# Performance work log

Measured on AMD Instinct MI355X. Metric: run time of the kernel, lower is better.

## Reference

```python
import jax, jax.numpy as jnp
import numpy as np

N_NODES = 100000
N_EDGES = 1200000
IN_CH = 64
HID = 64


def sage_conv(x, src, dst, Wl, b, Wr, num_nodes):
    # mean aggregation of source-node features at target nodes (flow=source_to_target)
    msg = x[src]                                      # [E, C] gather
    agg = jax.ops.segment_sum(msg, dst, num_segments=num_nodes)  # [N, C]
    cnt = jax.ops.segment_sum(jnp.ones((src.shape[0],), x.dtype), dst,
                              num_segments=num_nodes)
    mean = agg / jnp.maximum(cnt, 1.0)[:, None]
    # PyG SAGEConv: lin_l(aggregated) + bias + lin_r(root)
    return mean @ Wl + b + x @ Wr


def setup_inputs() -> dict:
    key = jax.random.key(0)
    ks = jax.random.split(key, 10)
    x = jax.random.normal(ks[0], (N_NODES, IN_CH), dtype=jnp.float32)
    edge_index = jax.random.randint(ks[1], (2, N_EDGES), 0, N_NODES, dtype=jnp.int64)
    s1 = 1.0 / np.sqrt(IN_CH)
    s2 = 1.0 / np.sqrt(HID)
    W1l = jax.random.uniform(ks[2], (IN_CH, HID), jnp.float32, -s1, s1)
    b1 = jax.random.uniform(ks[3], (HID,), jnp.float32, -s1, s1)
    W1r = jax.random.uniform(ks[4], (IN_CH, HID), jnp.float32, -s1, s1)
    W2l = jax.random.uniform(ks[5], (HID, HID), jnp.float32, -s2, s2)
    b2 = jax.random.uniform(ks[6], (HID,), jnp.float32, -s2, s2)
    W2r = jax.random.uniform(ks[7], (HID, HID), jnp.float32, -s2, s2)
    Wfc = jax.random.uniform(ks[8], (HID, 1), jnp.float32, -s2, s2)
    bfc = jax.random.uniform(ks[9], (1,), jnp.float32, -s2, s2)
    return {"x": x, "edge_index": edge_index, "W1l": W1l, "b1": b1, "W1r": W1r,
            "W2l": W2l, "b2": b2, "W2r": W2r, "Wfc": Wfc, "bfc": bfc}


def reference(x, edge_index, W1l, b1, W1r, W2l, b2, W2r, Wfc, bfc):
    num_nodes = x.shape[0]
    src, dst = edge_index[0], edge_index[1]
    x = jnp.nan_to_num(x, nan=0.0)
    # layer 1: SAGEConv -> ReLU (dropout is identity in eval)
    h = jax.nn.relu(sage_conv(x, src, dst, W1l, b1, W1r, num_nodes))
    # layer 2
    h = jax.nn.relu(sage_conv(h, src, dst, W2l, b2, W2r, num_nodes))
    pred = (h @ Wfc + bfc)[:, 0]  # (num_nodes,)
    return pred
```

## Files before the change

### kernel.cpp

```cpp
#include <hip/hip_runtime.h>

#define NN_NODES 100000
#define NN_EDGES 1200000
#define CH 64
#define BUCKET_NODES 200
#define NBUCKETS (NN_NODES / BUCKET_NODES)
#define EPB 4096
#define PREP_THREADS 1024
#define XCDS 8
#define PCAP 768
#define BMAX (XCDS * PCAP)

#define PA_BLOCKS ((NN_EDGES + EPB - 1) / EPB)
#define CV_ITEMS (NN_NODES * CH / 4)
#define CV_BLOCKS ((CV_ITEMS + PREP_THREADS - 1) / PREP_THREADS)
#define WP_ITEMS (64 * 128)
#define WP_BLOCKS ((WP_ITEMS + PREP_THREADS - 1) / PREP_THREADS)

#define FUSED_NODES 16
#define FUSED_BLOCKS (NN_NODES / FUSED_NODES)

typedef __attribute__((ext_vector_type(8))) short bf16x8;
typedef __attribute__((ext_vector_type(4))) float f32x4;

__device__ __forceinline__ float nan0(float v) { return v == v ? v : 0.0f; }

__device__ __forceinline__ unsigned short f2bf(float f) {
    unsigned u = __float_as_uint(f);
    return (unsigned short)((u + 0x7fffu + ((u >> 16) & 1u)) >> 16);
}

__device__ __forceinline__ unsigned xcc_id() {
    unsigned x;
    asm volatile("s_getreg_b32 %0, hwreg(HW_REG_XCC_ID)" : "=s"(x));
    return x & (XCDS - 1);
}

__global__ __launch_bounds__(PREP_THREADS) void prep_kernel(
    const float* __restrict__ x, unsigned short* __restrict__ xb,
    const float* __restrict__ W1l, const float* __restrict__ W1r,
    const float* __restrict__ W2l, const float* __restrict__ W2r,
    unsigned short* __restrict__ Wt1, unsigned short* __restrict__ Wt2,
    const int* __restrict__ src, const int* __restrict__ dst,
    int* __restrict__ bcnt, unsigned int* __restrict__ bbuf)
{
    __shared__ int lhist[NBUCKETS];
    __shared__ int lbase[NBUCKETS];
    int tid = threadIdx.x;
    int bid = blockIdx.x;

    if (bid < PA_BLOCKS) {
        int e0 = bid * EPB;
        unsigned xcc = xcc_id();

        for (int i = tid; i < NBUCKETS; i += PREP_THREADS) lhist[i] = 0;
        __syncthreads();

        int eb = e0 + tid * 4;
        int nv = NN_EDGES - eb;
        if (nv > 4) nv = 4;
        int da[4] = {-1, -1, -1, -1};
        if (nv == 4) {
            int4 dv = *(const int4*)(dst + eb);
            da[0] = dv.x; da[1] = dv.y; da[2] = dv.z; da[3] = dv.w;
        } else {
            for (int r = 0; r < nv; r++) da[r] = dst[eb + r];
        }
        #pragma unroll
        for (int r = 0; r < 4; r++)
            if (da[r] >= 0) atomicAdd(&lhist[da[r] / BUCKET_NODES], 1);
        __syncthreads();

        for (int i = tid; i < NBUCKETS; i += PREP_THREADS) {
            int c = lhist[i];
            lbase[i] = c > 0 ? atomicAdd(&bcnt[i * XCDS + xcc], c) : 0;
            lhist[i] = 0;
        }
        __syncthreads();

        int sa[4] = {0, 0, 0, 0};
        if (nv == 4) {
            int4 sv = *(const int4*)(src + eb);
            sa[0] = sv.x; sa[1] = sv.y; sa[2] = sv.z; sa[3] = sv.w;
        } else {
            for (int r = 0; r < nv; r++) sa[r] = src[eb + r];
        }
        #pragma unroll
        for (int r = 0; r < 4; r++) {
            int d = da[r];
            if (d >= 0) {
                int b = d / BUCKET_NODES;
                int dloc = d - b * BUCKET_NODES;
                int pos = lbase[b] + atomicAdd(&lhist[b], 1);
                if (pos < PCAP)
                    bbuf[((size_t)b * XCDS + xcc) * PCAP + pos] =
                        ((unsigned)dloc << 24) | (unsigned)sa[r];
            }
        }
    } else if (bid < PA_BLOCKS + CV_BLOCKS) {
        int i = (bid - PA_BLOCKS) * PREP_THREADS + tid;
        if (i < CV_ITEMS) {
            float4 v = ((const float4*)x)[i];
            v.x = nan0(v.x); v.y = nan0(v.y); v.z = nan0(v.z); v.w = nan0(v.w);
            ushort4 o;
            o.x = f2bf(v.x); o.y = f2bf(v.y); o.z = f2bf(v.z); o.w = f2bf(v.w);
            ((ushort4*)xb)[i] = o;
        }
    } else {
        int i = (bid - PA_BLOCKS - CV_BLOCKS) * PREP_THREADS + tid;
        if (i < WP_ITEMS) {
            int n = i >> 7;
            int k = i & 127;
            float v1 = (k < 64) ? W1l[k * 64 + n] : W1r[(k - 64) * 64 + n];
            float v2 = (k < 64) ? W2l[k * 64 + n] : W2r[(k - 64) * 64 + n];
            Wt1[i] = f2bf(v1);
            Wt2[i] = f2bf(v2);
        }
    }
}

__global__ __launch_bounds__(256) void passB_kernel(
    const int* __restrict__ bcnt, const unsigned int* __restrict__ bbuf,
    int* __restrict__ col, int* __restrict__ rowptr)
{
    __shared__ int hist[BUCKET_NODES];
    __shared__ int cur[BUCKET_NODES];
    __shared__ int sc[256];
    __shared__ unsigned int stage[BMAX];
    int b = blockIdx.x;
    int t = threadIdx.x;

    for (int i = t; i < BUCKET_NODES; i += 256) hist[i] = 0;

    int part = 0;
    int lim = b * XCDS;
    for (int i = t; i < lim; i += 256) {
        int c = bcnt[i];
        part += c > PCAP ? PCAP : c;
    }
    sc[t] = part;
    __syncthreads();
    #pragma unroll
    for (int off = 128; off > 0; off >>= 1) {
        if (t < off) sc[t] += sc[t + off];
        __syncthreads();
    }
    int base = sc[0];
    __syncthreads();

    int cnt = 0;
    #pragma unroll
    for (int x = 0; x < XCDS; x++) {
        int pc = bcnt[b * XCDS + x];
        if (pc > PCAP) pc = PCAP;
        const unsigned int* seg = bbuf + ((size_t)b * XCDS + x) * PCAP;
        for (int k = t; k < pc; k += 256) {
            unsigned v = seg[k];
            stage[cnt + k] = v;
            atomicAdd(&hist[v >> 24], 1);
        }
        cnt += pc;
    }
    __syncthreads();

    int own = (t < BUCKET_NODES) ? hist[t] : 0;
    sc[t] = own;
    __syncthreads();
    for (int off = 1; off < 256; off <<= 1) {
        int v = (t >= off) ? sc[t - off] : 0;
        __syncthreads();
        sc[t] += v;
        __syncthreads();
    }
    if (t < BUCKET_NODES) {
        int excl = sc[t] - own;
        rowptr[b * BUCKET_NODES + t] = base + excl;
        cur[t] = excl;
    }
    if (b == NBUCKETS - 1 && t == 0) rowptr[NN_NODES] = base + cnt;
    __syncthreads();

    for (int k = t; k < cnt; k += 256) {
        unsigned v = stage[k];
        int dloc = (int)(v >> 24);
        int pos = atomicAdd(&cur[dloc], 1);
        col[base + pos] = (int)(v & 0xFFFFFFu);
    }
}

template<int LAYER>
__global__ __launch_bounds__(256) void fused_kernel(
    const unsigned short* __restrict__ feat,
    const int* __restrict__ rowptr, const int* __restrict__ col,
    const unsigned short* __restrict__ Wt,
    const float* __restrict__ bias,
    const float* __restrict__ Wfc, const float* __restrict__ bfc,
    unsigned short* __restrict__ hb_out,
    float* __restrict__ out)
{
    __shared__ unsigned short sA[FUSED_NODES][136];
    __shared__ unsigned short sO[FUSED_NODES][72];
    __shared__ float psum[FUSED_NODES];

    int tid = threadIdx.x;
    int n_base = blockIdx.x * FUSED_NODES;

    int w    = tid >> 6;
    int lane = tid & 63;
    int quad = lane >> 4;
    int colx = lane & 15;

    for (int i = tid; i < FUSED_NODES * 8; i += 256) {
        int node = i >> 3;
        int c = i & 7;
        *(uint4*)&sA[node][64 + c * 8] =
            *(const uint4*)(feat + (size_t)(n_base + node) * CH + c * 8);
    }
    if (LAYER == 2 && tid < FUSED_NODES) psum[tid] = 0.f;

    int r0a[4], r1a[4];
    #pragma unroll
    for (int j = 0; j < 4; j++) {
        int node = n_base + w * 4 + j;
        r0a[j] = rowptr[node];
        r1a[j] = rowptr[node + 1];
    }

    int sidx[4][4];
    #pragma unroll
    for (int j = 0; j < 4; j++) {
        int r1 = r1a[j];
        int bi = r0a[j] + quad;
        #pragma unroll
        for (int m = 0; m < 4; m++) {
            int idx = bi + 4 * m;
            sidx[j][m] = col[idx < r1 ? idx : 0];
        }
    }

    uint2 u[4][4];
    #pragma unroll
    for (int j = 0; j < 4; j++) {
        #pragma unroll
        for (int m = 0; m < 4; m++) {
            u[j][m] = *(const uint2*)(feat + (size_t)sidx[j][m] * CH + colx * 4);
        }
    }

    #pragma unroll
    for (int j = 0; j < 4; j++) {
        int nl = w * 4 + j;
        int r0 = r0a[j], r1 = r1a[j];
        float a0[4] = {0, 0, 0, 0};
        #pragma unroll
        for (int m = 0; m < 4; m++) {
            if (r0 + quad + 4 * m < r1) {
                a0[0] += __uint_as_float(u[j][m].x << 16);
                a0[1] += __uint_as_float(u[j][m].x & 0xffff0000u);
                a0[2] += __uint_as_float(u[j][m].y << 16);
                a0[3] += __uint_as_float(u[j][m].y & 0xffff0000u);
            }
        }
        int i = r0 + quad + 16;
        if (i < r1) {
            float b0[4] = {0, 0, 0, 0}, b1[4] = {0, 0, 0, 0};
            for (; i + 4 < r1; i += 8) {
                int s0 = col[i];
                int s1 = col[i + 4];
                uint2 v0 = *(const uint2*)(feat + (size_t)s0 * CH + colx * 4);
                uint2 v1 = *(const uint2*)(feat + (size_t)s1 * CH + colx * 4);
                b0[0] += __uint_as_float(v0.x << 16);
                b0[1] += __uint_as_float(v0.x & 0xffff0000u);
                b0[2] += __uint_as_float(v0.y << 16);
                b0[3] += __uint_as_float(v0.y & 0xffff0000u);
                b1[0] += __uint_as_float(v1.x << 16);
                b1[1] += __uint_as_float(v1.x & 0xffff0000u);
                b1[2] += __uint_as_float(v1.y << 16);
                b1[3] += __uint_as_float(v1.y & 0xffff0000u);
            }
            if (i < r1) {
                int s0 = col[i];
                uint2 v0 = *(const uint2*)(feat + (size_t)s0 * CH + colx * 4);
                b0[0] += __uint_as_float(v0.x << 16);
                b0[1] += __uint_as_float(v0.x & 0xffff0000u);
                b0[2] += __uint_as_float(v0.y << 16);
                b0[3] += __uint_as_float(v0.y & 0xffff0000u);
            }
            #pragma unroll
            for (int q = 0; q < 4; q++) a0[q] += b0[q] + b1[q];
        }
        #pragma unroll
        for (int q = 0; q < 4; q++) {
            a0[q] += __shfl_xor(a0[q], 16, 64);
            a0[q] += __shfl_xor(a0[q], 32, 64);
        }
        if (lane < 16) {
            int deg = r1 - r0;
            float inv = 1.0f / (float)(deg > 0 ? deg : 1);
            ushort4 o;
            o.x = f2bf(a0[0] * inv); o.y = f2bf(a0[1] * inv);
            o.z = f2bf(a0[2] * inv); o.w = f2bf(a0[3] * inv);
            *(ushort4*)&sA[nl][colx * 4] = o;
        }
    }
    __syncthreads();

    const unsigned short* wrow = Wt + (size_t)(w * 16 + colx) * 128;
    float bv = bias[w * 16 + colx];

    f32x4 acc = (f32x4){0.f, 0.f, 0.f, 0.f};
    #pragma unroll
    for (int ks = 0; ks < 4; ks++) {
        bf16x8 bfr = *(const bf16x8*)(wrow + ks * 32 + quad * 8);
        bf16x8 af = *(const bf16x8*)&sA[colx][ks * 32 + quad * 8];
        acc = __builtin_amdgcn_mfma_f32_16x16x32_bf16(af, bfr, acc, 0, 0, 0);
    }

    if (LAYER == 1) {
        #pragma unroll
        for (int r = 0; r < 4; r++) {
            float v = acc[r] + bv;
            v = v > 0.f ? v : 0.f;
            sO[quad * 4 + r][w * 16 + colx] = f2bf(v);
        }
        __syncthreads();
        for (int i = tid; i < FUSED_NODES * 8; i += 256) {
            int node = i >> 3;
            int c = i & 7;
            *(uint4*)(hb_out + (size_t)(n_base + node) * CH + c * 8) =
                *(const uint4*)&sO[node][c * 8];
        }
    } else {
        float wf = Wfc[w * 16 + colx];
        #pragma unroll
        for (int r = 0; r < 4; r++) {
            float v = acc[r] + bv;
            v = v > 0.f ? v : 0.f;
            float p = v * wf;
            p += __shfl_xor(p, 1, 64);
            p += __shfl_xor(p, 2, 64);
            p += __shfl_xor(p, 4, 64);
            p += __shfl_xor(p, 8, 64);
            if (colx == 0) atomicAdd(&psum[quad * 4 + r], p);
        }
        __syncthreads();
        if (tid < FUSED_NODES) out[n_base + tid] = psum[tid] + bfc[0];
    }
}

extern "C" void kernel_launch(void* const* d_in, const int* in_sizes, int n_in,
                              void* d_out, int out_size, void* d_ws, size_t ws_size,
                              hipStream_t stream) {
    const float* x    = (const float*)d_in[0];
    const int*   ei   = (const int*)d_in[1];
    const float* W1l  = (const float*)d_in[2];
    const float* b1   = (const float*)d_in[3];
    const float* W1r  = (const float*)d_in[4];
    const float* W2l  = (const float*)d_in[5];
    const float* b2   = (const float*)d_in[6];
    const float* W2r  = (const float*)d_in[7];
    const float* Wfc  = (const float*)d_in[8];
    const float* bfc  = (const float*)d_in[9];
    float* out = (float*)d_out;

    const int N = NN_NODES;
    const int E = NN_EDGES;
    const int* src = ei;
    const int* dst = ei + E;

    char* ws = (char*)d_ws;
    unsigned short* xb  = (unsigned short*)ws;  ws += (size_t)N * CH * sizeof(unsigned short);
    unsigned short* h1b = (unsigned short*)ws;  ws += (size_t)N * CH * sizeof(unsigned short);
    unsigned short* Wt1 = (unsigned short*)ws;  ws += 64 * 128 * sizeof(unsigned short);
    unsigned short* Wt2 = (unsigned short*)ws;  ws += 64 * 128 * sizeof(unsigned short);
    int* bcnt   = (int*)ws;                     ws += (size_t)NBUCKETS * XCDS * sizeof(int);
    int* rowptr = (int*)ws;                     ws += (size_t)(N + 1) * sizeof(int);
    int* col    = (int*)ws;                     ws += (size_t)E * sizeof(int);
    unsigned int* bbuf = (unsigned int*)ws;     ws += (size_t)NBUCKETS * XCDS * PCAP * sizeof(unsigned int);

    hipMemsetAsync(bcnt, 0, (size_t)NBUCKETS * XCDS * sizeof(int), stream);

    prep_kernel<<<PA_BLOCKS + CV_BLOCKS + WP_BLOCKS, PREP_THREADS, 0, stream>>>(
        x, xb, W1l, W1r, W2l, W2r, Wt1, Wt2, src, dst, bcnt, bbuf);
    passB_kernel<<<NBUCKETS, 256, 0, stream>>>(bcnt, bbuf, col, rowptr);

    fused_kernel<1><<<FUSED_BLOCKS, 256, 0, stream>>>(
        xb, rowptr, col, Wt1, b1, nullptr, nullptr, h1b, nullptr);
    fused_kernel<2><<<FUSED_BLOCKS, 256, 0, stream>>>(
        h1b, rowptr, col, Wt2, b2, Wfc, bfc, nullptr, out);
}
```

Measured before the change: 196.4 us.

## Drop CSR build pass and filter bucketed edges inside fused kernels

Removes the separate passB kernel that turned per-bucket edge buffers into a CSR rowptr/col layout. Each fused block now scans the bucket segments covering its 16 nodes and keeps only edges whose destination falls in its range. It appends their sources to a shared-memory list via LDS atomics, then gathers from that list. This saves a kernel launch and the col/rowptr writes and reads, but every bucket is now rescanned by many blocks in both layers, and per-node degree is capped at 128 entries.

```diff
diff --git a/kernel.cpp b/kernel.cpp
--- a/kernel.cpp
+++ b/kernel.cpp
@@ -9,7 +9,6 @@
 #define PREP_THREADS 1024
 #define XCDS 8
 #define PCAP 768
-#define BMAX (XCDS * PCAP)
 
 #define PA_BLOCKS ((NN_EDGES + EPB - 1) / EPB)
 #define CV_ITEMS (NN_NODES * CH / 4)
@@ -19,6 +18,7 @@
 
 #define FUSED_NODES 16
 #define FUSED_BLOCKS (NN_NODES / FUSED_NODES)
+#define ELIST_CAP 128
 
 typedef __attribute__((ext_vector_type(8))) short bf16x8;
 typedef __attribute__((ext_vector_type(4))) float f32x4;
@@ -119,79 +119,10 @@
     }
 }
 
-__global__ __launch_bounds__(256) void passB_kernel(
-    const int* __restrict__ bcnt, const unsigned int* __restrict__ bbuf,
-    int* __restrict__ col, int* __restrict__ rowptr)
-{
-    __shared__ int hist[BUCKET_NODES];
-    __shared__ int cur[BUCKET_NODES];
-    __shared__ int sc[256];
-    __shared__ unsigned int stage[BMAX];
-    int b = blockIdx.x;
-    int t = threadIdx.x;
-
-    for (int i = t; i < BUCKET_NODES; i += 256) hist[i] = 0;
-
-    int part = 0;
-    int lim = b * XCDS;
-    for (int i = t; i < lim; i += 256) {
-        int c = bcnt[i];
-        part += c > PCAP ? PCAP : c;
-    }
-    sc[t] = part;
-    __syncthreads();
-    #pragma unroll
-    for (int off = 128; off > 0; off >>= 1) {
-        if (t < off) sc[t] += sc[t + off];
-        __syncthreads();
-    }
-    int base = sc[0];
-    __syncthreads();
-
-    int cnt = 0;
-    #pragma unroll
-    for (int x = 0; x < XCDS; x++) {
-        int pc = bcnt[b * XCDS + x];
-        if (pc > PCAP) pc = PCAP;
-        const unsigned int* seg = bbuf + ((size_t)b * XCDS + x) * PCAP;
-        for (int k = t; k < pc; k += 256) {
-            unsigned v = seg[k];
-            stage[cnt + k] = v;
-            atomicAdd(&hist[v >> 24], 1);
-        }
-        cnt += pc;
-    }
-    __syncthreads();
-
-    int own = (t < BUCKET_NODES) ? hist[t] : 0;
-    sc[t] = own;
-    __syncthreads();
-    for (int off = 1; off < 256; off <<= 1) {
-        int v = (t >= off) ? sc[t - off] : 0;
-        __syncthreads();
-        sc[t] += v;
-        __syncthreads();
-    }
-    if (t < BUCKET_NODES) {
-        int excl = sc[t] - own;
-        rowptr[b * BUCKET_NODES + t] = base + excl;
-        cur[t] = excl;
-    }
-    if (b == NBUCKETS - 1 && t == 0) rowptr[NN_NODES] = base + cnt;
-    __syncthreads();
-
-    for (int k = t; k < cnt; k += 256) {
-        unsigned v = stage[k];
-        int dloc = (int)(v >> 24);
-        int pos = atomicAdd(&cur[dloc], 1);
-        col[base + pos] = (int)(v & 0xFFFFFFu);
-    }
-}
-
 template<int LAYER>
 __global__ __launch_bounds__(256) void fused_kernel(
     const unsigned short* __restrict__ feat,
-    const int* __restrict__ rowptr, const int* __restrict__ col,
+    const int* __restrict__ bcnt, const unsigned int* __restrict__ bbuf,
     const unsigned short* __restrict__ Wt,
     const float* __restrict__ bias,
     const float* __restrict__ Wfc, const float* __restrict__ bfc,
@@ -201,6 +132,8 @@
     __shared__ unsigned short sA[FUSED_NODES][136];
     __shared__ unsigned short sO[FUSED_NODES][72];
     __shared__ float psum[FUSED_NODES];
+    __shared__ int elist[FUSED_NODES][ELIST_CAP];
+    __shared__ int ecnt[FUSED_NODES];
 
     int tid = threadIdx.x;
     int n_base = blockIdx.x * FUSED_NODES;
@@ -210,31 +143,58 @@
     int quad = lane >> 4;
     int colx = lane & 15;
 
+    if (tid < FUSED_NODES) {
+        ecnt[tid] = 0;
+        psum[tid] = 0.f;
+    }
     for (int i = tid; i < FUSED_NODES * 8; i += 256) {
         int node = i >> 3;
         int c = i & 7;
         *(uint4*)&sA[node][64 + c * 8] =
             *(const uint4*)(feat + (size_t)(n_base + node) * CH + c * 8);
     }
-    if (LAYER == 2 && tid < FUSED_NODES) psum[tid] = 0.f;
-
-    int r0a[4], r1a[4];
+    __syncthreads();
+
+    {
+        int bA = n_base / BUCKET_NODES;
+        int bB = (n_base + FUSED_NODES - 1) / BUCKET_NODES;
+        for (int bkt = bA; bkt <= bB; bkt++) {
+            int boff = bkt * BUCKET_NODES;
+            #pragma unroll
+            for (int x = 0; x < XCDS; x++) {
+                int pc = bcnt[bkt * XCDS + x];
+                if (pc > PCAP) pc = PCAP;
+                const unsigned int* seg = bbuf + ((size_t)bkt * XCDS + x) * PCAP;
+                for (int k = tid; k < pc; k += 256) {
+                    unsigned v = seg[k];
+                    unsigned rel = (unsigned)(boff + (int)(v >> 24) - n_base);
+                    if (rel < (unsigned)FUSED_NODES) {
+                        int slot = atomicAdd(&ecnt[rel], 1);
+                        if (slot < ELIST_CAP)
+                            elist[rel][slot] = (int)(v & 0xFFFFFFu);
+                    }
+                }
+            }
+        }
+    }
+    __syncthreads();
+
+    int dega[4];
     #pragma unroll
     for (int j = 0; j < 4; j++) {
-        int node = n_base + w * 4 + j;
-        r0a[j] = rowptr[node];
-        r1a[j] = rowptr[node + 1];
+        int d = ecnt[w * 4 + j];
+        dega[j] = d < ELIST_CAP ? d : ELIST_CAP;
     }
 
     int sidx[4][4];
     #pragma unroll
     for (int j = 0; j < 4; j++) {
-        int r1 = r1a[j];
-        int bi = r0a[j] + quad;
+        int nl = w * 4 + j;
         #pragma unroll
         for (int m = 0; m < 4; m++) {
-            int idx = bi + 4 * m;
-            sidx[j][m] = col[idx < r1 ? idx : 0];
+            int slot = quad + 4 * m;
+            int sv = elist[nl][slot];
+            sidx[j][m] = slot < dega[j] ? sv : 0;
         }
     }
 
@@ -250,23 +210,23 @@
     #pragma unroll
     for (int j = 0; j < 4; j++) {
         int nl = w * 4 + j;
-        int r0 = r0a[j], r1 = r1a[j];
+        int deg = dega[j];
         float a0[4] = {0, 0, 0, 0};
         #pragma unroll
         for (int m = 0; m < 4; m++) {
-            if (r0 + quad + 4 * m < r1) {
+            if (quad + 4 * m < deg) {
                 a0[0] += __uint_as_float(u[j][m].x << 16);
                 a0[1] += __uint_as_float(u[j][m].x & 0xffff0000u);
                 a0[2] += __uint_as_float(u[j][m].y << 16);
                 a0[3] += __uint_as_float(u[j][m].y & 0xffff0000u);
             }
         }
-        int i = r0 + quad + 16;
-        if (i < r1) {
+        int i = quad + 16;
+        if (i < deg) {
             float b0[4] = {0, 0, 0, 0}, b1[4] = {0, 0, 0, 0};
-            for (; i + 4 < r1; i += 8) {
-                int s0 = col[i];
-                int s1 = col[i + 4];
+            for (; i + 4 < deg; i += 8) {
+                int s0 = elist[nl][i];
+                int s1 = elist[nl][i + 4];
                 uint2 v0 = *(const uint2*)(feat + (size_t)s0 * CH + colx * 4);
                 uint2 v1 = *(const uint2*)(feat + (size_t)s1 * CH + colx * 4);
                 b0[0] += __uint_as_float(v0.x << 16);
@@ -278,8 +238,8 @@
                 b1[2] += __uint_as_float(v1.y << 16);
                 b1[3] += __uint_as_float(v1.y & 0xffff0000u);
             }
-            if (i < r1) {
-                int s0 = col[i];
+            if (i < deg) {
+                int s0 = elist[nl][i];
                 uint2 v0 = *(const uint2*)(feat + (size_t)s0 * CH + colx * 4);
                 b0[0] += __uint_as_float(v0.x << 16);
                 b0[1] += __uint_as_float(v0.x & 0xffff0000u);
@@ -295,7 +255,6 @@
             a0[q] += __shfl_xor(a0[q], 32, 64);
         }
         if (lane < 16) {
-            int deg = r1 - r0;
             float inv = 1.0f / (float)(deg > 0 ? deg : 1);
             ushort4 o;
             o.x = f2bf(a0[0] * inv); o.y = f2bf(a0[1] * inv);
@@ -374,18 +333,15 @@
     unsigned short* Wt1 = (unsigned short*)ws;  ws += 64 * 128 * sizeof(unsigned short);
     unsigned short* Wt2 = (unsigned short*)ws;  ws += 64 * 128 * sizeof(unsigned short);
     int* bcnt   = (int*)ws;                     ws += (size_t)NBUCKETS * XCDS * sizeof(int);
-    int* rowptr = (int*)ws;                     ws += (size_t)(N + 1) * sizeof(int);
-    int* col    = (int*)ws;                     ws += (size_t)E * sizeof(int);
     unsigned int* bbuf = (unsigned int*)ws;     ws += (size_t)NBUCKETS * XCDS * PCAP * sizeof(unsigned int);
 
     hipMemsetAsync(bcnt, 0, (size_t)NBUCKETS * XCDS * sizeof(int), stream);
 
     prep_kernel<<<PA_BLOCKS + CV_BLOCKS + WP_BLOCKS, PREP_THREADS, 0, stream>>>(
         x, xb, W1l, W1r, W2l, W2r, Wt1, Wt2, src, dst, bcnt, bbuf);
-    passB_kernel<<<NBUCKETS, 256, 0, stream>>>(bcnt, bbuf, col, rowptr);
 
     fused_kernel<1><<<FUSED_BLOCKS, 256, 0, stream>>>(
-        xb, rowptr, col, Wt1, b1, nullptr, nullptr, h1b, nullptr);
+        xb, bcnt, bbuf, Wt1, b1, nullptr, nullptr, h1b, nullptr);
     fused_kernel<2><<<FUSED_BLOCKS, 256, 0, stream>>>(
-        h1b, rowptr, col, Wt2, b2, Wfc, bfc, nullptr, out);
-}
+        h1b, bcnt, bbuf, Wt2, b2, Wfc, bfc, nullptr, out);
+}
```

After: 224.6 us. 14.3% more time.
